# Performance work log

Hardware: AMD Instinct MI355X
Metric: run time of the kernel (lower is better)

The kernel has to match this reference:

```python
import jax, jax.numpy as jnp
import numpy as np

IN_DIM, DIM, G, B = 512, 1024, 16, 4096

def _gelu(x):
    return jax.nn.gelu(x, approximate=False)  # torch nn.GELU default = exact erf


def setup_inputs() -> dict:
    key = jax.random.key(0)
    ks = jax.random.split(key, 11)
    sc_in = 1.0 / np.sqrt(IN_DIM)
    sc_d = 1.0 / np.sqrt(DIM)
    return {
        "x": jax.random.normal(ks[0], (B, IN_DIM), dtype=jnp.float32),
        "genre": jax.random.randint(ks[1], (B,), 0, G),
        # shared MLP params
        "W1": jax.random.uniform(ks[2], (IN_DIM, DIM), jnp.float32, -sc_in, sc_in),
        "b1": jax.random.uniform(ks[3], (DIM,), jnp.float32, -sc_in, sc_in),
        "W2": jax.random.uniform(ks[4], (DIM, DIM), jnp.float32, -sc_d, sc_d),
        "b2": jax.random.uniform(ks[5], (DIM,), jnp.float32, -sc_d, sc_d),
        # unshared (per-genre) MLP params, stacked over experts
        "Wa": jax.random.uniform(ks[6], (G, DIM, DIM), jnp.float32, -sc_d, sc_d),
        "ba": jax.random.uniform(ks[7], (G, DIM), jnp.float32, -sc_d, sc_d),
        "Wb": jax.random.uniform(ks[8], (G, DIM, DIM), jnp.float32, -sc_d, sc_d),
        "bb": jax.random.uniform(ks[9], (G, DIM), jnp.float32, -sc_d, sc_d),
    }


def reference(x, genre, W1, b1, W2, b2, Wa, ba, Wb, bb):
    # shared trunk: Linear -> GELU -> Linear -> GELU
    s = _gelu(_gelu(x @ W1 + b1) @ W2 + b2)          # [B, D]
    # dense per-genre expert branches (faithful to original: compute all, then gather)
    h = _gelu(jnp.einsum('bd,gde->bge', s, Wa) + ba[None, :, :])  # [B, G, D]
    out_all = jnp.einsum('bgd,gde->bge', h, Wb) + bb[None, :, :]  # [B, G, D]
    # gather each sample's own genre branch
    return jnp.take_along_axis(out_all, genre[:, None, None], axis=1)[:, 0, :]  # [B, D]
```

## Files before the change

### kernel.cpp

```cpp
#include <hip/hip_runtime.h>
#include <hip/hip_bf16.h>
#include <math.h>

#define BATCH 4096
#define INDIM 512
#define NDIM  1024
#define NG    16

typedef __bf16 bf16_t;
typedef __bf16 bf16x8 __attribute__((ext_vector_type(8)));
typedef float  f32x4  __attribute__((ext_vector_type(4)));
typedef unsigned int u32;
typedef unsigned int u32x4 __attribute__((ext_vector_type(4)));

__device__ __forceinline__ float gelu_exact(float v) {
    return 0.5f * v * (1.0f + erff(v * 0.70710678118654752440f));
}

__device__ __forceinline__ void gload_lds16(const void* g, void* l) {
    __builtin_amdgcn_global_load_lds((const __attribute__((address_space(1))) void*)g,
                                     (__attribute__((address_space(3))) void*)l,
                                     16, 0, 0);
}

__device__ __forceinline__ u32 pkbf(float a, float b) {
    union { bf16_t h[2]; u32 v; } x;
    x.h[0] = (bf16_t)a; x.h[1] = (bf16_t)b;
    return x.v;
}

__global__ __launch_bounds__(256)
void build_perm_kernel(const int* __restrict__ genre,
                       int* __restrict__ perm,
                       int* __restrict__ offsets ) {
    __shared__ int cc[64][NG];
    __shared__ int gtot[NG];
    __shared__ int goff[NG];
    const int t = threadIdx.x;
    for (int i = t; i < 64 * NG; i += 256) (&cc[0][0])[i] = 0;
    __syncthreads();
    if (t < 64) {
        #pragma unroll 1
        for (int i = 0; i < 64; ++i) {
            int g = genre[t * 64 + i] & (NG - 1);
            cc[t][g] += 1;
        }
    }
    __syncthreads();
    if (t < NG) {
        int s = 0;
        #pragma unroll 1
        for (int c = 0; c < 64; ++c) { int v = cc[c][t]; cc[c][t] = s; s += v; }
        gtot[t] = s;
    }
    __syncthreads();
    if (t == 0) {
        int s = 0;
        for (int g = 0; g < NG; ++g) { goff[g] = s; offsets[g] = s; s += gtot[g]; }
        offsets[NG] = s;
    }
    __syncthreads();
    if (t < 64) {
        #pragma unroll 1
        for (int i = 0; i < 64; ++i) {
            int b = t * 64 + i;
            int g = genre[b] & (NG - 1);
            int pos = goff[g] + cc[t][g];
            cc[t][g] += 1;
            perm[pos] = b;
        }
    }
}

__global__ __launch_bounds__(256)
void convert_x_kernel(const float* __restrict__ src, bf16_t* __restrict__ dst) {
    const int i = (blockIdx.x * 256 + threadIdx.x) * 8;
    float4 a = *(const float4*)&src[i];
    float4 b = *(const float4*)&src[i + 4];
    bf16x8 w;
    w[0] = (bf16_t)a.x; w[1] = (bf16_t)a.y; w[2] = (bf16_t)a.z; w[3] = (bf16_t)a.w;
    w[4] = (bf16_t)b.x; w[5] = (bf16_t)b.y; w[6] = (bf16_t)b.z; w[7] = (bf16_t)b.w;
    *(bf16x8*)&dst[i] = w;
}

__device__ __forceinline__ void transpose_tile64(const float* __restrict__ src,
                                                 bf16_t* __restrict__ dst,
                                                 int K, int N, int k0, int n0, int t) {
    __shared__ u32 T[64][34];
    const int kp_l = t >> 4;
    const int nc   = (t & 15) * 4;
    #pragma unroll
    for (int iter = 0; iter < 2; ++iter) {
        const int kr = iter * 32 + kp_l * 2;
        const float* p0 = src + (size_t)(k0 + kr) * N + n0 + nc;
        float4 r0 = *(const float4*)p0;
        float4 r1 = *(const float4*)(p0 + N);
        const int kp = iter * 16 + kp_l;
        T[nc + 0][kp] = pkbf(r0.x, r1.x);
        T[nc + 1][kp] = pkbf(r0.y, r1.y);
        T[nc + 2][kp] = pkbf(r0.z, r1.z);
        T[nc + 3][kp] = pkbf(r0.w, r1.w);
    }
    __syncthreads();
    const int n  = t >> 2;
    const int c8 = (t & 3) * 8;
    u32 v[8];
    #pragma unroll
    for (int j = 0; j < 8; ++j) v[j] = T[n][c8 + j];
    u32* d = (u32*)((char*)dst + ((size_t)(n0 + n) * K + k0) * 2) + c8;
    *(u32x4*)(d)     = (u32x4){v[0], v[1], v[2], v[3]};
    *(u32x4*)(d + 4) = (u32x4){v[4], v[5], v[6], v[7]};
}

__global__ __launch_bounds__(256)
void transpose_w_kernel(const float* __restrict__ src, bf16_t* __restrict__ dst,
                        int K, int N) {
    const size_t slab = (size_t)blockIdx.z * (size_t)K * (size_t)N;
    transpose_tile64(src + slab, dst + slab, K, N, blockIdx.x * 64, blockIdx.y * 64,
                     threadIdx.x);
}

__global__ __launch_bounds__(256)
void transpose_w2_kernel(const float* __restrict__ srcA, bf16_t* __restrict__ dstA,
                         const float* __restrict__ srcB, bf16_t* __restrict__ dstB) {
    const int z = blockIdx.z;
    const size_t slab = (size_t)(z & 15) * NDIM * NDIM;
    const float* s = (z < 16 ? srcA : srcB) + slab;
    bf16_t*      d = (z < 16 ? dstA : dstB) + slab;
    transpose_tile64(s, d, NDIM, NDIM, blockIdx.x * 64, blockIdx.y * 64, threadIdx.x);
}

template<bool EXPERT, bool GATHER_A, bool GELU_OUT, bool SCATTER_OUT, bool OUT_BF16>
__global__ __launch_bounds__(1024, 4)
void gemm128_kernel(const bf16_t* __restrict__ A,
                    const bf16_t* __restrict__ Bt,
                    const float* __restrict__ bias,
                    void* __restrict__ Cout,
                    int K,
                    const int* __restrict__ perm,
                    const int* __restrict__ offsets) {
    constexpr int N = NDIM;
    __shared__ bf16_t As[2][128 * 64];
    __shared__ bf16_t Bs[2][128 * 64];

    const int n0 = blockIdx.y * 128;
    int m0 = 0, mloc0 = 0, count = 1 << 30, gbase = 0;
    const bf16_t* Bp = Bt;
    const float* biasp = bias;

    if constexpr (EXPERT) {
        const int bx = blockIdx.x;
        int g = 0, accum = 0, cnt = 0;
        for (; g < NG; ++g) {
            cnt = offsets[g + 1] - offsets[g];
            int nt = (cnt + 127) >> 7;
            if (bx < accum + nt) break;
            accum += nt;
        }
        if (g >= NG) return;
        count = cnt;
        mloc0 = (bx - accum) * 128;
        gbase = offsets[g];
        m0 = gbase + mloc0;
        Bp = Bt + (size_t)g * N * NDIM;
        biasp = bias + g * N;
    } else {
        m0 = blockIdx.x * 128;
    }

    const int tid  = threadIdx.x;
    const int wave = tid >> 6;
    const int lane = tid & 63;
    const int l15  = lane & 15;
    const int l16  = lane >> 4;
    const int wr   = wave >> 2;
    const int wc   = wave & 3;

    const int srow   = tid >> 3;
    const int srcoff = (((tid & 7) ^ ((tid >> 3) & 7)) * 16);
    int arow;
    if constexpr (EXPERT) {
        int rcl = mloc0 + srow;
        if (rcl >= count) rcl = count - 1;
        arow = GATHER_A ? perm[gbase + rcl] : (gbase + rcl);
    } else {
        arow = m0 + srow;
    }
    const char* aptr = (const char*)(A + (size_t)arow * K) + srcoff;
    const char* bptr = (const char*)(Bp + (size_t)(n0 + srow) * K) + srcoff;

    f32x4 acc[2][2];
    #pragma unroll
    for (int m = 0; m < 2; ++m)
        #pragma unroll
        for (int n = 0; n < 2; ++n)
            acc[m][n] = (f32x4){0.f, 0.f, 0.f, 0.f};

    const int nsteps = K >> 6;
    const int w1024 = wave * 1024;

    auto stage = [&](int buf, int t) {
        const size_t ko = (size_t)t * 128;
        gload_lds16(aptr + ko, (char*)&As[buf][0] + w1024);
        gload_lds16(bptr + ko, (char*)&Bs[buf][0] + w1024);
    };

    stage(0, 0);
    int cur = 0;
    for (int t = 0; t < nsteps; ++t) {
        if (t + 1 < nsteps) {
            stage(cur ^ 1, t + 1);
            asm volatile("s_waitcnt vmcnt(2)" ::: "memory");
        } else {
            asm volatile("s_waitcnt vmcnt(0)" ::: "memory");
        }
        asm volatile("s_barrier" ::: "memory");

        #pragma unroll
        for (int kk = 0; kk < 2; ++kk) {
            bf16x8 a[2], b[2];
            #pragma unroll
            for (int m = 0; m < 2; ++m) {
                const int row = wr * 32 + m * 16 + l15;
                const int chunk = (kk * 4 + l16) ^ (lane & 7);
                a[m] = *(const bf16x8*)&As[cur][row * 64 + chunk * 8];
            }
            #pragma unroll
            for (int n = 0; n < 2; ++n) {
                const int row = wc * 32 + n * 16 + l15;
                const int chunk = (kk * 4 + l16) ^ (lane & 7);
                b[n] = *(const bf16x8*)&Bs[cur][row * 64 + chunk * 8];
            }
            #pragma unroll
            for (int m = 0; m < 2; ++m)
                #pragma unroll
                for (int n = 0; n < 2; ++n)
                    acc[m][n] = __builtin_amdgcn_mfma_f32_16x16x32_bf16(a[m], b[n], acc[m][n], 0, 0, 0);
        }
        asm volatile("s_barrier" ::: "memory");
        cur ^= 1;
    }

    #pragma unroll
    for (int n = 0; n < 2; ++n) {
        const int col = n0 + wc * 32 + n * 16 + l15;
        const float bv = biasp[col];
        #pragma unroll
        for (int m = 0; m < 2; ++m) {
            #pragma unroll
            for (int r = 0; r < 4; ++r) {
                const int row_local = wr * 32 + m * 16 + l16 * 4 + r;
                if constexpr (EXPERT) {
                    if (mloc0 + row_local >= count) continue;
                }
                float v = acc[m][n][r] + bv;
                if constexpr (GELU_OUT) v = gelu_exact(v);
                int orow = m0 + row_local;
                if constexpr (SCATTER_OUT) orow = perm[orow];
                if constexpr (OUT_BF16)
                    ((bf16_t*)Cout)[(size_t)orow * N + col] = (bf16_t)v;
                else
                    ((float*)Cout)[(size_t)orow * N + col] = v;
            }
        }
    }
}

extern "C" void kernel_launch(void* const* d_in, const int* in_sizes, int n_in,
                              void* d_out, int out_size, void* d_ws, size_t ws_size,
                              hipStream_t stream) {
    const float* x     = (const float*)d_in[0];
    const int*   genre = (const int*)  d_in[1];
    const float* W1    = (const float*)d_in[2];
    const float* b1    = (const float*)d_in[3];
    const float* W2    = (const float*)d_in[4];
    const float* b2    = (const float*)d_in[5];
    const float* Wa    = (const float*)d_in[6];
    const float* ba    = (const float*)d_in[7];
    const float* Wb    = (const float*)d_in[8];
    const float* bb    = (const float*)d_in[9];
    float* out = (float*)d_out;

    char* ws = (char*)d_ws;
    const size_t MB = 1 << 20;
    bf16_t* W1t = (bf16_t*)(ws);
    bf16_t* W2t = (bf16_t*)(ws + 1 * MB);
    bf16_t* Wat = (bf16_t*)(ws + 3 * MB);
    bf16_t* Wbt = (bf16_t*)(ws + 35 * MB);
    bf16_t* xb  = (bf16_t*)(ws + 67 * MB);
    bf16_t* s1b = (bf16_t*)(ws + 71 * MB);
    bf16_t* sb  = (bf16_t*)(ws + 79 * MB);
    int*    perm    = (int*)(ws + 87 * MB);
    int*    offsets = (int*)(ws + 87 * MB + 65536);
    bf16_t* hb = s1b;

    build_perm_kernel<<<1, 256, 0, stream>>>(genre, perm, offsets);
    convert_x_kernel<<<BATCH * INDIM / (256 * 8), 256, 0, stream>>>(x, xb);
    transpose_w_kernel<<<dim3(INDIM / 64, NDIM / 64, 1), 256, 0, stream>>>(W1, W1t, INDIM, NDIM);
    transpose_w_kernel<<<dim3(NDIM / 64, NDIM / 64, 1),  256, 0, stream>>>(W2, W2t, NDIM, NDIM);
    transpose_w2_kernel<<<dim3(NDIM / 64, NDIM / 64, 2 * NG), 256, 0, stream>>>(
        Wa, Wat, Wb, Wbt);

    gemm128_kernel<false, false, true, false, true><<<dim3(32, 8), 1024, 0, stream>>>(
        xb, W1t, b1, s1b, INDIM, nullptr, nullptr);
    gemm128_kernel<false, false, true, false, true><<<dim3(32, 8), 1024, 0, stream>>>(
        s1b, W2t, b2, sb, NDIM, nullptr, nullptr);
    gemm128_kernel<true, true, true, false, true><<<dim3(48, 8), 1024, 0, stream>>>(
        sb, Wat, ba, hb, NDIM, perm, offsets);
    gemm128_kernel<true, false, false, true, false><<<dim3(48, 8), 1024, 0, stream>>>(
        hb, Wbt, bb, out, NDIM, perm, offsets);
}
```

Baseline: 146.8 us.

## Transpose weights in per-block K strips with double-buffered register prefetch

```diff
diff --git a/kernel.cpp b/kernel.cpp
--- a/kernel.cpp
+++ b/kernel.cpp
@@ -83,51 +83,94 @@
     *(bf16x8*)&dst[i] = w;
 }
 
-__device__ __forceinline__ void transpose_tile64(const float* __restrict__ src,
-                                                 bf16_t* __restrict__ dst,
-                                                 int K, int N, int k0, int n0, int t) {
-    __shared__ u32 T[64][34];
+template<int K>
+struct TStrip {
+    u32 T[2][64][34];
+};
+
+template<int K>
+__device__ __forceinline__ void transpose_strip_body(const float* __restrict__ src,
+                                                     bf16_t* __restrict__ dst,
+                                                     int N, int n0, int t) {
+    __shared__ u32 T[2][64][34];
+    constexpr int NT = K / 64;
+
     const int kp_l = t >> 4;
     const int nc   = (t & 15) * 4;
+    const int kr0  = kp_l * 2;
+    const int n    = t >> 2;
+    const int c8   = (t & 3) * 8;
+
+    f32x4 ra[4], rb[4];
+
+    auto load = [&](f32x4* r, int kt) {
+        const float* p = src + (size_t)(kt * 64 + kr0) * N + n0 + nc;
+        r[0] = *(const f32x4*)p;
+        r[1] = *(const f32x4*)(p + N);
+        r[2] = *(const f32x4*)(p + 32 * N);
+        r[3] = *(const f32x4*)(p + 33 * N);
+        __builtin_amdgcn_sched_barrier(0);
+    };
+    auto pack = [&](const f32x4* r, int buf) {
+        T[buf][nc + 0][kp_l]      = pkbf(r[0][0], r[1][0]);
+        T[buf][nc + 1][kp_l]      = pkbf(r[0][1], r[1][1]);
+        T[buf][nc + 2][kp_l]      = pkbf(r[0][2], r[1][2]);
+        T[buf][nc + 3][kp_l]      = pkbf(r[0][3], r[1][3]);
+        T[buf][nc + 0][16 + kp_l] = pkbf(r[2][0], r[3][0]);
+        T[buf][nc + 1][16 + kp_l] = pkbf(r[2][1], r[3][1]);
+        T[buf][nc + 2][16 + kp_l] = pkbf(r[2][2], r[3][2]);
+        T[buf][nc + 3][16 + kp_l] = pkbf(r[2][3], r[3][3]);
+    };
+    auto flush = [&](int buf, int kt) {
+        u32 v[8];
+        #pragma unroll
+        for (int j = 0; j < 8; ++j) v[j] = T[buf][n][c8 + j];
+        u32* d = (u32*)((char*)dst + ((size_t)(n0 + n) * K + kt * 64) * 2) + c8;
+        *(u32x4*)(d)     = (u32x4){v[0], v[1], v[2], v[3]};
+        *(u32x4*)(d + 4) = (u32x4){v[4], v[5], v[6], v[7]};
+    };
+
+    auto step = [&](int kt, f32x4* cur, f32x4* nxt) {
+        const int buf = kt & 1;
+        if (kt + 1 < NT) load(nxt, kt + 1);
+        if (kt == 0) {
+            if (NT > 1) asm volatile("s_waitcnt vmcnt(4)" ::: "memory");
+            else        asm volatile("s_waitcnt vmcnt(0)" ::: "memory");
+        } else if (kt + 1 < NT) {
+            asm volatile("s_waitcnt vmcnt(6)" ::: "memory");
+        } else {
+            asm volatile("s_waitcnt vmcnt(2)" ::: "memory");
+        }
+        pack(cur, buf);
+        asm volatile("s_waitcnt lgkmcnt(0)" ::: "memory");
+        asm volatile("s_barrier" ::: "memory");
+        flush(buf, kt);
+    };
+
+    load(ra, 0);
     #pragma unroll
-    for (int iter = 0; iter < 2; ++iter) {
-        const int kr = iter * 32 + kp_l * 2;
-        const float* p0 = src + (size_t)(k0 + kr) * N + n0 + nc;
-        float4 r0 = *(const float4*)p0;
-        float4 r1 = *(const float4*)(p0 + N);
-        const int kp = iter * 16 + kp_l;
-        T[nc + 0][kp] = pkbf(r0.x, r1.x);
-        T[nc + 1][kp] = pkbf(r0.y, r1.y);
-        T[nc + 2][kp] = pkbf(r0.z, r1.z);
-        T[nc + 3][kp] = pkbf(r0.w, r1.w);
-    }
-    __syncthreads();
-    const int n  = t >> 2;
-    const int c8 = (t & 3) * 8;
-    u32 v[8];
-    #pragma unroll
-    for (int j = 0; j < 8; ++j) v[j] = T[n][c8 + j];
-    u32* d = (u32*)((char*)dst + ((size_t)(n0 + n) * K + k0) * 2) + c8;
-    *(u32x4*)(d)     = (u32x4){v[0], v[1], v[2], v[3]};
-    *(u32x4*)(d + 4) = (u32x4){v[4], v[5], v[6], v[7]};
-}
-
+    for (int kt = 0; kt < NT; kt += 2) {
+        step(kt, ra, rb);
+        step(kt + 1, rb, ra);
+    }
+}
+
+template<int K>
 __global__ __launch_bounds__(256)
-void transpose_w_kernel(const float* __restrict__ src, bf16_t* __restrict__ dst,
-                        int K, int N) {
+void transpose_strip_kernel(const float* __restrict__ src, bf16_t* __restrict__ dst,
+                            int N) {
     const size_t slab = (size_t)blockIdx.z * (size_t)K * (size_t)N;
-    transpose_tile64(src + slab, dst + slab, K, N, blockIdx.x * 64, blockIdx.y * 64,
-                     threadIdx.x);
+    transpose_strip_body<K>(src + slab, dst + slab, N, blockIdx.x * 64, threadIdx.x);
 }
 
 __global__ __launch_bounds__(256)
-void transpose_w2_kernel(const float* __restrict__ srcA, bf16_t* __restrict__ dstA,
-                         const float* __restrict__ srcB, bf16_t* __restrict__ dstB) {
+void transpose_strip2_kernel(const float* __restrict__ srcA, bf16_t* __restrict__ dstA,
+                             const float* __restrict__ srcB, bf16_t* __restrict__ dstB) {
     const int z = blockIdx.z;
     const size_t slab = (size_t)(z & 15) * NDIM * NDIM;
     const float* s = (z < 16 ? srcA : srcB) + slab;
     bf16_t*      d = (z < 16 ? dstA : dstB) + slab;
-    transpose_tile64(s, d, NDIM, NDIM, blockIdx.x * 64, blockIdx.y * 64, threadIdx.x);
+    transpose_strip_body<NDIM>(s, d, NDIM, blockIdx.x * 64, threadIdx.x);
 }
 
 template<bool EXPERT, bool GATHER_A, bool GELU_OUT, bool SCATTER_OUT, bool OUT_BF16>
@@ -296,9 +339,9 @@
 
     build_perm_kernel<<<1, 256, 0, stream>>>(genre, perm, offsets);
     convert_x_kernel<<<BATCH * INDIM / (256 * 8), 256, 0, stream>>>(x, xb);
-    transpose_w_kernel<<<dim3(INDIM / 64, NDIM / 64, 1), 256, 0, stream>>>(W1, W1t, INDIM, NDIM);
-    transpose_w_kernel<<<dim3(NDIM / 64, NDIM / 64, 1),  256, 0, stream>>>(W2, W2t, NDIM, NDIM);
-    transpose_w2_kernel<<<dim3(NDIM / 64, NDIM / 64, 2 * NG), 256, 0, stream>>>(
+    transpose_strip_kernel<INDIM><<<dim3(NDIM / 64, 1, 1), 256, 0, stream>>>(W1, W1t, NDIM);
+    transpose_strip_kernel<NDIM><<<dim3(NDIM / 64, 1, 1), 256, 0, stream>>>(W2, W2t, NDIM);
+    transpose_strip2_kernel<<<dim3(NDIM / 64, 1, 2 * NG), 256, 0, stream>>>(
         Wa, Wat, Wb, Wbt);
 
     gemm128_kernel<false, false, true, false, true><<<dim3(32, 8), 1024, 0, stream>>>(
```

After: 149.7 us. 1.02x slower.

## Transpose weights in pipelined K-strips with triple-buffered register prefetch

Applied to the files above, without the earlier changes.

```diff
diff --git a/kernel.cpp b/kernel.cpp
--- a/kernel.cpp
+++ b/kernel.cpp
@@ -83,51 +83,82 @@
     *(bf16x8*)&dst[i] = w;
 }
 
-__device__ __forceinline__ void transpose_tile64(const float* __restrict__ src,
-                                                 bf16_t* __restrict__ dst,
-                                                 int K, int N, int k0, int n0, int t) {
-    __shared__ u32 T[64][34];
+template<int NT>
+__device__ __forceinline__ void transpose_strip_body(const float* __restrict__ src,
+                                                     bf16_t* __restrict__ dst,
+                                                     int N, int K, int n0, int kbase,
+                                                     int t) {
+    __shared__ u32 T[2][64][34];
+
     const int kp_l = t >> 4;
     const int nc   = (t & 15) * 4;
+    const int kr0  = kp_l * 2;
+    const int n    = t >> 2;
+    const int c8   = (t & 3) * 8;
+
+    f32x4 r[3][4];
+
+    auto load = [&](int slot, int kt) {
+        const float* p = src + (size_t)(kbase + kt * 64 + kr0) * N + n0 + nc;
+        r[slot][0] = *(const f32x4*)p;
+        r[slot][1] = *(const f32x4*)(p + N);
+        r[slot][2] = *(const f32x4*)(p + 32 * N);
+        r[slot][3] = *(const f32x4*)(p + 33 * N);
+        __builtin_amdgcn_sched_barrier(0);
+    };
+    auto pack = [&](int slot, int buf) {
+        T[buf][nc + 0][kp_l]      = pkbf(r[slot][0][0], r[slot][1][0]);
+        T[buf][nc + 1][kp_l]      = pkbf(r[slot][0][1], r[slot][1][1]);
+        T[buf][nc + 2][kp_l]      = pkbf(r[slot][0][2], r[slot][1][2]);
+        T[buf][nc + 3][kp_l]      = pkbf(r[slot][0][3], r[slot][1][3]);
+        T[buf][nc + 0][16 + kp_l] = pkbf(r[slot][2][0], r[slot][3][0]);
+        T[buf][nc + 1][16 + kp_l] = pkbf(r[slot][2][1], r[slot][3][1]);
+        T[buf][nc + 2][16 + kp_l] = pkbf(r[slot][2][2], r[slot][3][2]);
+        T[buf][nc + 3][16 + kp_l] = pkbf(r[slot][2][3], r[slot][3][3]);
+    };
+    auto flush = [&](int buf, int kt) {
+        u32 v[8];
+        #pragma unroll
+        for (int j = 0; j < 8; ++j) v[j] = T[buf][n][c8 + j];
+        u32* d = (u32*)((char*)dst + ((size_t)(n0 + n) * K + kbase + kt * 64) * 2) + c8;
+        *(u32x4*)(d)     = (u32x4){v[0], v[1], v[2], v[3]};
+        *(u32x4*)(d + 4) = (u32x4){v[4], v[5], v[6], v[7]};
+    };
+
+    load(0, 0);
+    load(1, 1);
     #pragma unroll
-    for (int iter = 0; iter < 2; ++iter) {
-        const int kr = iter * 32 + kp_l * 2;
-        const float* p0 = src + (size_t)(k0 + kr) * N + n0 + nc;
-        float4 r0 = *(const float4*)p0;
-        float4 r1 = *(const float4*)(p0 + N);
-        const int kp = iter * 16 + kp_l;
-        T[nc + 0][kp] = pkbf(r0.x, r1.x);
-        T[nc + 1][kp] = pkbf(r0.y, r1.y);
-        T[nc + 2][kp] = pkbf(r0.z, r1.z);
-        T[nc + 3][kp] = pkbf(r0.w, r1.w);
-    }
-    __syncthreads();
-    const int n  = t >> 2;
-    const int c8 = (t & 3) * 8;
-    u32 v[8];
-    #pragma unroll
-    for (int j = 0; j < 8; ++j) v[j] = T[n][c8 + j];
-    u32* d = (u32*)((char*)dst + ((size_t)(n0 + n) * K + k0) * 2) + c8;
-    *(u32x4*)(d)     = (u32x4){v[0], v[1], v[2], v[3]};
-    *(u32x4*)(d + 4) = (u32x4){v[4], v[5], v[6], v[7]};
-}
-
+    for (int kt = 0; kt < NT; ++kt) {
+        if (kt + 2 < NT) load((kt + 2) % 3, kt + 2);
+        if (kt == 0)           asm volatile("s_waitcnt vmcnt(8)"  ::: "memory");
+        else if (kt + 2 < NT)  asm volatile("s_waitcnt vmcnt(10)" ::: "memory");
+        else if (kt + 1 < NT)  asm volatile("s_waitcnt vmcnt(6)"  ::: "memory");
+        else                   asm volatile("s_waitcnt vmcnt(2)"  ::: "memory");
+        pack(kt % 3, kt & 1);
+        asm volatile("s_waitcnt lgkmcnt(0)" ::: "memory");
+        asm volatile("s_barrier" ::: "memory");
+        flush(kt & 1, kt);
+    }
+}
+
+template<int NT>
 __global__ __launch_bounds__(256)
-void transpose_w_kernel(const float* __restrict__ src, bf16_t* __restrict__ dst,
-                        int K, int N) {
+void transpose_strip_kernel(const float* __restrict__ src, bf16_t* __restrict__ dst,
+                            int N, int K) {
     const size_t slab = (size_t)blockIdx.z * (size_t)K * (size_t)N;
-    transpose_tile64(src + slab, dst + slab, K, N, blockIdx.x * 64, blockIdx.y * 64,
-                     threadIdx.x);
+    transpose_strip_body<NT>(src + slab, dst + slab, N, K, blockIdx.x * 64,
+                             blockIdx.y * (NT * 64), threadIdx.x);
 }
 
 __global__ __launch_bounds__(256)
-void transpose_w2_kernel(const float* __restrict__ srcA, bf16_t* __restrict__ dstA,
-                         const float* __restrict__ srcB, bf16_t* __restrict__ dstB) {
+void transpose_strip2_kernel(const float* __restrict__ srcA, bf16_t* __restrict__ dstA,
+                             const float* __restrict__ srcB, bf16_t* __restrict__ dstB) {
     const int z = blockIdx.z;
     const size_t slab = (size_t)(z & 15) * NDIM * NDIM;
     const float* s = (z < 16 ? srcA : srcB) + slab;
     bf16_t*      d = (z < 16 ? dstA : dstB) + slab;
-    transpose_tile64(s, d, NDIM, NDIM, blockIdx.x * 64, blockIdx.y * 64, threadIdx.x);
+    transpose_strip_body<NDIM / 128>(s, d, NDIM, NDIM, blockIdx.x * 64,
+                                     blockIdx.y * (NDIM / 2), threadIdx.x);
 }
 
 template<bool EXPERT, bool GATHER_A, bool GELU_OUT, bool SCATTER_OUT, bool OUT_BF16>
@@ -296,9 +327,11 @@
 
     build_perm_kernel<<<1, 256, 0, stream>>>(genre, perm, offsets);
     convert_x_kernel<<<BATCH * INDIM / (256 * 8), 256, 0, stream>>>(x, xb);
-    transpose_w_kernel<<<dim3(INDIM / 64, NDIM / 64, 1), 256, 0, stream>>>(W1, W1t, INDIM, NDIM);
-    transpose_w_kernel<<<dim3(NDIM / 64, NDIM / 64, 1),  256, 0, stream>>>(W2, W2t, NDIM, NDIM);
-    transpose_w2_kernel<<<dim3(NDIM / 64, NDIM / 64, 2 * NG), 256, 0, stream>>>(
+    transpose_strip_kernel<INDIM / 128><<<dim3(NDIM / 64, 2, 1), 256, 0, stream>>>(
+        W1, W1t, NDIM, INDIM);
+    transpose_strip_kernel<NDIM / 128><<<dim3(NDIM / 64, 2, 1), 256, 0, stream>>>(
+        W2, W2t, NDIM, NDIM);
+    transpose_strip2_kernel<<<dim3(NDIM / 64, 2, 2 * NG), 256, 0, stream>>>(
         Wa, Wat, Wb, Wbt);
 
     gemm128_kernel<false, false, true, false, true><<<dim3(32, 8), 1024, 0, stream>>>(
```

After: 148.9 us. Within noise of the previous version (+1.4%).
